# Performance work log

Hardware: AMD Instinct MI355X
Metric: run time of the kernel (lower is better)

## Reference

```python
import jax, jax.numpy as jnp
import numpy as np

B, C, T, W, H = 4, 128, 16, 64, 64


def setup_inputs() -> dict:
    key = jax.random.key(0)
    ks = jax.random.split(key, 5)
    Cq = C // 8
    return {
        "x": jax.random.normal(ks[0], (B, C, T, W, H), jnp.float32),
        # stacked params for the 3 cells (T, W, H order, as in nn.Sequential)
        "Wq": jax.random.normal(ks[1], (3, Cq, C), jnp.float32) * 0.05,
        "bq": jnp.zeros((3, Cq), jnp.float32),
        "Wk": jax.random.normal(ks[2], (3, Cq, C), jnp.float32) * 0.05,
        "bk": jnp.zeros((3, Cq), jnp.float32),
        "Wv": jax.random.normal(ks[3], (3, C, C), jnp.float32) * 0.05,
        "bv": jnp.zeros((3, C), jnp.float32),
        # gamma is init to 0 in torch (identity); small random so the test is nontrivial
        "gamma": jax.random.normal(ks[4], (3,), jnp.float32) * 0.1,
    }


def _conv1x1(x, w, b):
    # 1x1x1 Conv3d == channel contraction
    return jnp.einsum('bcthw,oc->bothw', x, w) + b[None, :, None, None, None]


def _cell(x, wq, bq, wk, bk, wv, bv, gamma, attn_dim):
    # Faithful to torch: raw contiguous .view() == row-major reshape.
    Bb, Cc, Tt, Ww, Hh = x.shape
    q = _conv1x1(x, wq, bq).reshape(Bb, attn_dim, -1)   # (B, A, N)
    k = _conv1x1(x, wk, bk).reshape(Bb, -1, attn_dim)   # (B, N, A)  (pooling_factor=1 -> MaxPool identity)
    attn = jax.nn.softmax(jnp.matmul(q, k), axis=-1)    # (B, A, A)
    v = _conv1x1(x, wv, bv).reshape(Bb, -1, attn_dim)   # (B, M, A), M = C*T*W*H/A
    out = jnp.matmul(v, attn.swapaxes(1, 2))            # (B, M, A)
    out = out.reshape(Bb, Cc, Ww, Hh, Tt).transpose(0, 1, 4, 2, 3)  # -> (B, C, T, W, H)
    return gamma * out + x


def reference(x, Wq, bq, Wk, bk, Wv, bv, gamma):
    _, _, Tt, Ww, Hh = x.shape
    attn_dims = (Tt, Ww, Hh)  # cells with attn_id 'T', 'W', 'H'
    for i in range(3):
        x = _cell(x, Wq[i], bq[i], Wk[i], bk[i], Wv[i], bv[i], gamma[i], attn_dims[i])
    return x
```

## Files before the change

kernel.cpp:

```cpp
#include <hip/hip_runtime.h>

#define BB 4
#define CC 128
#define CQ 16
#define TDIM 16
#define SS 65536
#define CS (CC*SS)
#define NBLK 256

typedef unsigned short u16;
typedef unsigned int   u32;

typedef __bf16 bf16x8v __attribute__((ext_vector_type(8)));
typedef float  floatx4v __attribute__((ext_vector_type(4)));

__device__ __forceinline__ u16 f2bf(float f) {
    u32 u = __float_as_uint(f);
    u32 r = (u + 0x7fffu + ((u >> 16) & 1u)) >> 16;
    return (u16)r;
}
__device__ __forceinline__ void unpack8(uint4 r, float* f) {
    f[0] = __uint_as_float(r.x << 16); f[1] = __uint_as_float(r.x & 0xffff0000u);
    f[2] = __uint_as_float(r.y << 16); f[3] = __uint_as_float(r.y & 0xffff0000u);
    f[4] = __uint_as_float(r.z << 16); f[5] = __uint_as_float(r.z & 0xffff0000u);
    f[6] = __uint_as_float(r.w << 16); f[7] = __uint_as_float(r.w & 0xffff0000u);
}
__device__ __forceinline__ bf16x8v ld_bf8(const void* p) {
    union { uint4 u; bf16x8v b; } x;
    x.u = *(const uint4*)p;
    return x.b;
}

__global__ __launch_bounds__(256) void wconv_kernel(
    const float* __restrict__ Wq, const float* __restrict__ Wk, const float* __restrict__ Wv,
    const float* __restrict__ bq, const float* __restrict__ bk, const float* __restrict__ bv,
    u16* __restrict__ wbf, float* __restrict__ bias)
{
    const int idx = blockIdx.x * 256 + threadIdx.x;
    const int cell = idx / 20480;
    const int j = idx - cell * 20480;
    const int o = j >> 7, c = j & 127;
    float v;
    if (o < 16)      v = Wq[(cell * 16 + o) * 128 + c];
    else if (o < 32) v = Wk[(cell * 16 + (o - 16)) * 128 + c];
    else             v = Wv[(cell * 128 + (o - 32)) * 128 + c];
    wbf[idx] = f2bf(v);
    if (idx < 480) {
        const int cl = idx / 160, oo = idx - cl * 160;
        float b = (oo < 16) ? bq[cl * 16 + oo]
                : (oo < 32) ? bk[cl * 16 + oo - 16]
                :             bv[cl * 128 + oo - 32];
        bias[idx] = b;
    }
}

__global__ __launch_bounds__(512, 4) void qkv_mfma_kernel(
    const float* __restrict__ x,
    const u16* __restrict__ wbf, const float* __restrict__ bias,
    float* __restrict__ qf, float* __restrict__ kf, u16* __restrict__ vf)
{
    __shared__ u16 xT[128 * 128];
    const int t  = threadIdx.x;
    const int b  = blockIdx.y;
    const int s0 = blockIdx.x << 7;
    const float* xb = x + (size_t)b * CS;

    {
        const int s4 = (t & 31) << 2;
        const int cr = t >> 5;
        const float* xs = xb + s0 + s4;
#pragma unroll
        for (int p = 0; p < 8; p++) {
            const int c = cr + p * 16;
            float4 f = *(const float4*)(xs + (size_t)c * SS);
            u16 h[4] = { f2bf(f.x), f2bf(f.y), f2bf(f.z), f2bf(f.w) };
#pragma unroll
            for (int j = 0; j < 4; j++) {
                const int sl = s4 + j;
                const u32 sw = (u32)(((sl & 7) ^ ((sl >> 3) & 7)) << 4);
                *(u16*)((char*)xT + ((((u32)sl << 8) + ((u32)c << 1)) ^ sw)) = h[j];
            }
        }
    }
    __syncthreads();

    const int lane = t & 63;
    const int wv   = t >> 6;
    const int mh   = wv >> 2;
    const int sq   = wv & 3;
    const int ln15 = lane & 15;
    const int lhi  = lane >> 4;

    floatx4v acc[5][2] = {};

    const u16* abase = wbf + ((mh * 80 + ln15) << 7) + (lhi << 3);

#pragma unroll
    for (int ks = 0; ks < 4; ks++) {
        bf16x8v af[5];
#pragma unroll
        for (int mi = 0; mi < 5; mi++)
            af[mi] = ld_bf8(abase + (mi << 11) + (ks << 5));
#pragma unroll
        for (int nt = 0; nt < 2; nt++) {
            const int sl = sq * 32 + nt * 16 + ln15;
            const u32 sw = (u32)(((sl & 7) ^ ((sl >> 3) & 7)) << 4);
            const u32 off = (((u32)sl << 8) + (u32)((ks << 6) + (lhi << 4))) ^ sw;
            bf16x8v bf = ld_bf8((const char*)xT + off);
#pragma unroll
            for (int mi = 0; mi < 5; mi++)
                acc[mi][nt] = __builtin_amdgcn_mfma_f32_16x16x32_bf16(
                                  af[mi], bf, acc[mi][nt], 0, 0, 0);
        }
    }

    float* qb = qf + (size_t)b * ((size_t)CQ * SS);
    float* kb = kf + (size_t)b * ((size_t)CQ * SS);
    u16*   vb = vf + (size_t)b * (size_t)CS;

    if (mh == 0) {
#pragma unroll
        for (int mi = 0; mi < 2; mi++) {
            const int o0 = mi * 16 + lhi * 4;
            float bia[4];
            *(float4*)bia = *(const float4*)(bias + o0);
            float* base = (mi == 0) ? qb : kb;
            const int row0 = o0 & 15;
#pragma unroll
            for (int nt = 0; nt < 2; nt++) {
                const int s = s0 + sq * 32 + nt * 16 + ln15;
#pragma unroll
                for (int r = 0; r < 4; r++)
                    base[(size_t)(row0 + r) * SS + s] = acc[mi][nt][r] + bia[r];
            }
        }
    }
    __syncthreads();

#pragma unroll
    for (int mi = 0; mi < 5; mi++) {
        const int o0 = mh * 80 + mi * 16 + lhi * 4;
        if (o0 >= 32) {
            float bia[4];
            *(float4*)bia = *(const float4*)(bias + o0);
            const int vc0 = o0 - 32;
#pragma unroll
            for (int nt = 0; nt < 2; nt++) {
                const int sl = sq * 32 + nt * 16 + ln15;
#pragma unroll
                for (int r = 0; r < 4; r++) {
                    const int vc = vc0 + r;
                    const u32 sw = (u32)(((vc & 7) ^ ((vc >> 3) & 7)) << 4);
                    *(u16*)((char*)xT + ((((u32)vc << 8) + ((u32)sl << 1)) ^ sw))
                        = f2bf(acc[mi][nt][r] + bia[r]);
                }
            }
        }
    }
    __syncthreads();

#pragma unroll
    for (int it = 0; it < 4; it++) {
        const int vc = (t >> 4) + it * 32;
        const u32 sw = (u32)(((vc & 7) ^ ((vc >> 3) & 7)) << 4);
        uint4 d = *(const uint4*)((char*)xT +
                      ((((u32)vc << 8) + ((u32)(t & 15) << 4)) ^ sw));
        *(uint4*)(vb + (size_t)vc * SS + s0 + ((t & 15) << 3)) = d;
    }
}

template <int A>
__global__ __launch_bounds__(256) void logits_part_kernel(
    const float* __restrict__ qf, const float* __restrict__ kf,
    float* __restrict__ part)
{
    constexpr int N = (CQ * SS) / A;
    constexpr int NCHUNK = N / NBLK;
    constexpr int NLOG = (NCHUNK == 64) ? 6 : 8;
    __shared__ float qs[A][NCHUNK + 1];
    __shared__ float ks[NCHUNK][A];
    const int t  = threadIdx.x;
    const int b  = blockIdx.y;
    const int n0 = blockIdx.x << NLOG;
    const float* qb = qf + (size_t)b * ((size_t)CQ * SS);
    const float* kb = kf + (size_t)b * ((size_t)CQ * SS);

    for (int idx = t; idx < A * NCHUNK; idx += 256) {
        int a1 = idx >> NLOG, n = idx & (NCHUNK - 1);
        qs[a1][n] = qb[(size_t)a1 * N + n0 + n];
    }
    float* ksf = &ks[0][0];
    for (int idx = t; idx < NCHUNK * A; idx += 256)
        ksf[idx] = kb[(size_t)n0 * A + idx];
    __syncthreads();

    float* pb = part + ((size_t)b * NBLK + blockIdx.x) * (A * A);

    if constexpr (A == 16) {
        int a1 = t >> 4, a2 = t & 15;
        float s = 0.f;
#pragma unroll 8
        for (int n = 0; n < NCHUNK; n++) s += qs[a1][n] * ks[n][a2];
        pb[t] = s;
    } else {
        int a1  = t & 63;
        int a2b = (t >> 6) * 16;
        float acc[16];
#pragma unroll
        for (int j = 0; j < 16; j++) acc[j] = 0.f;
        for (int n = 0; n < NCHUNK; n++) {
            float q = qs[a1][n];
#pragma unroll
            for (int j = 0; j < 16; j++) acc[j] += q * ks[n][a2b + j];
        }
        float* dst = pb + t * 16;
        *(float4*)(dst)      = make_float4(acc[0],  acc[1],  acc[2],  acc[3]);
        *(float4*)(dst + 4)  = make_float4(acc[4],  acc[5],  acc[6],  acc[7]);
        *(float4*)(dst + 8)  = make_float4(acc[8],  acc[9],  acc[10], acc[11]);
        *(float4*)(dst + 12) = make_float4(acc[12], acc[13], acc[14], acc[15]);
    }
}

template <int A>
__global__ __launch_bounds__(256) void reduce_softmax_kernel(
    const float* __restrict__ part, float* __restrict__ attn, u16* __restrict__ pbf)
{
    constexpr int NG = 256 / A;
    __shared__ float red[NG][A];
    const int a1 = blockIdx.x;
    const int b  = blockIdx.y;
    const int t  = threadIdx.x;
    const int a2 = t & (A - 1);
    const int g  = t >> ((A == 16) ? 4 : 6);
    const float* pb = part + (size_t)b * NBLK * (A * A);

    int off;
    if constexpr (A == 16) off = a1 * 16 + a2;
    else                   off = a1 * 16 + ((a2 >> 4) << 10) + (a2 & 15);

    float s0 = 0.f, s1 = 0.f, s2 = 0.f, s3 = 0.f;
    for (int blk = g; blk < NBLK; blk += 4 * NG) {
        s0 += pb[(size_t)(blk         ) * (A * A) + off];
        s1 += pb[(size_t)(blk +     NG) * (A * A) + off];
        s2 += pb[(size_t)(blk + 2 * NG) * (A * A) + off];
        s3 += pb[(size_t)(blk + 3 * NG) * (A * A) + off];
    }
    red[g][a2] = (s0 + s1) + (s2 + s3);
    __syncthreads();

    if (t < A) {
        float l = 0.f;
#pragma unroll
        for (int gg = 0; gg < NG; gg++) l += red[gg][t];
        float m = l;
#pragma unroll
        for (int o2 = A / 2; o2 > 0; o2 >>= 1) m = fmaxf(m, __shfl_xor(m, o2, 64));
        float e = expf(l - m);
        float s = e;
#pragma unroll
        for (int o2 = A / 2; o2 > 0; o2 >>= 1) s += __shfl_xor(s, o2, 64);
        const float p = e / s;
        attn[((size_t)b << 12) + a1 * A + t] = p;
        if constexpr (A == 64)
            pbf[((size_t)b << 12) + a1 * 64 + t] = f2bf(p);
    }
}

__global__ __launch_bounds__(256) void out16_kernel(
    const float* __restrict__ x, const u16* __restrict__ vf,
    const float* __restrict__ attn, const float* __restrict__ gptr,
    float* __restrict__ y)
{
    const int b = blockIdx.y;
    const u32 u = blockIdx.x * 256u + threadIdx.x;
    const float g = *gptr;
    const float* ab = attn + ((size_t)b << 12);
    const float* xb = x + (size_t)b * CS;
    float*       yb = y + (size_t)b * CS;
    const u16*   vr = vf + (size_t)b * CS + (size_t)u * 16;

    uint4 r0 = *(const uint4*)(vr);
    uint4 r1 = *(const uint4*)(vr + 8);
    float v0[8], v1[8];
    unpack8(r0, v0); unpack8(r1, v1);

    const size_t base = ((size_t)(u >> 12) << 16) + (u & 4095u);
#pragma unroll
    for (int tt = 0; tt < 16; tt++) {
        const float* ar = ab + tt * 16;
        float4 a0 = *(const float4*)(ar);
        float4 a1 = *(const float4*)(ar + 4);
        float4 a2 = *(const float4*)(ar + 8);
        float4 a3 = *(const float4*)(ar + 12);
        float acc = v0[0]*a0.x + v0[1]*a0.y + v0[2]*a0.z + v0[3]*a0.w
                  + v0[4]*a1.x + v0[5]*a1.y + v0[6]*a1.z + v0[7]*a1.w
                  + v1[0]*a2.x + v1[1]*a2.y + v1[2]*a2.z + v1[3]*a2.w
                  + v1[4]*a3.x + v1[5]*a3.y + v1[6]*a3.z + v1[7]*a3.w;
        const size_t i = base + ((size_t)tt << 12);
        yb[i] = g * acc + xb[i];
    }
}

__global__ __launch_bounds__(256) void out64_mfma_kernel(
    const float* __restrict__ x, const u16* __restrict__ vf,
    const u16* __restrict__ pbf, const float* __restrict__ gptr,
    float* __restrict__ y)
{
    const int b = blockIdx.y;
    const int t = threadIdx.x;
    const float g = *gptr;
    const int lane = t & 63;
    const int ln15 = lane & 15;
    const int lhi  = lane >> 4;
    const int wv   = t >> 6;
    const int m0w  = blockIdx.x * 256 + wv * 64;

    const u16*   pb = pbf + ((size_t)b << 12);
    const u16*   vb = vf + (size_t)b * CS;
    const float* xb = x + (size_t)b * CS;
    float*       yb = y + (size_t)b * CS;

    bf16x8v af[2][4];
#pragma unroll
    for (int ksi = 0; ksi < 2; ksi++)
#pragma unroll
        for (int sub = 0; sub < 4; sub++)
            af[ksi][sub] = ld_bf8(pb + (sub * 16 + ln15) * 64 + ksi * 32 + lhi * 8);

#pragma unroll
    for (int tile = 0; tile < 4; tile++) {
        const int m0 = m0w + tile * 16;
        const u16* vrow = vb + ((size_t)(m0 + ln15) << 6) + (lhi << 3);
        bf16x8v b0 = ld_bf8(vrow);
        bf16x8v b1 = ld_bf8(vrow + 32);

        floatx4v acc[4] = {};
#pragma unroll
        for (int sub = 0; sub < 4; sub++) {
            acc[sub] = __builtin_amdgcn_mfma_f32_16x16x32_bf16(af[0][sub], b0, acc[sub], 0, 0, 0);
            acc[sub] = __builtin_amdgcn_mfma_f32_16x16x32_bf16(af[1][sub], b1, acc[sub], 0, 0, 0);
        }

        const int c   = m0 >> 10;
        const int ow  = ((m0 >> 6) & 15) * 4 + ((m0 & 63) >> 4);
        const size_t base = ((size_t)c << 16) + ((size_t)ow << 6) + (size_t)(ln15 << 2);
        const float* xbase = xb + base;
        float*       ybase = yb + base;
#pragma unroll
        for (int r = 0; r < 4; r++) {
            const int ot = lhi * 4 + r;
            float4 xv = *(const float4*)(xbase + ((size_t)ot << 12));
            float4 o;
            o.x = g * acc[0][r] + xv.x;
            o.y = g * acc[1][r] + xv.y;
            o.z = g * acc[2][r] + xv.z;
            o.w = g * acc[3][r] + xv.w;
            *(float4*)(ybase + ((size_t)ot << 12)) = o;
        }
    }
}

extern "C" void kernel_launch(void* const* d_in, const int* in_sizes, int n_in,
                              void* d_out, int out_size, void* d_ws, size_t ws_size,
                              hipStream_t stream)
{
    (void)in_sizes; (void)n_in; (void)out_size;
    const float* x0    = (const float*)d_in[0];
    const float* Wq    = (const float*)d_in[1];
    const float* bq    = (const float*)d_in[2];
    const float* Wk    = (const float*)d_in[3];
    const float* bk    = (const float*)d_in[4];
    const float* Wv    = (const float*)d_in[5];
    const float* bv    = (const float*)d_in[6];
    const float* gamma = (const float*)d_in[7];
    float* y = (float*)d_out;

    const size_t MiB = (size_t)1 << 20;
    const size_t need4 = 4 * (28 * MiB + 16384 + 8192) + 160 * 128 * 3 * 2 + 3 * 160 * 4;
    const int nb = (ws_size >= need4) ? 4 : 1;

    char* ws = (char*)d_ws;
    float* qf    = (float*)ws;
    float* kf    = (float*)(ws + (size_t)nb * 4  * MiB);
    u16*   vf    = (u16*)  (ws + (size_t)nb * 8  * MiB);
    float* part  = (float*)(ws + (size_t)nb * 24 * MiB);
    float* attnp = (float*)(ws + (size_t)nb * 28 * MiB);
    u16*   pbf   = (u16*)  (ws + (size_t)nb * 28 * MiB + (size_t)nb * 16384);
    u16*   wbf3  = (u16*)  (ws + (size_t)nb * 28 * MiB + (size_t)nb * (16384 + 8192));
    float* bias3 = (float*)(ws + (size_t)nb * 28 * MiB + (size_t)nb * (16384 + 8192)
                               + 160 * 128 * 3 * 2);

    wconv_kernel<<<240, 256, 0, stream>>>(Wq, Wk, Wv, bq, bk, bv, wbf3, bias3);

    for (int cell = 0; cell < 3; cell++) {
        const u16*   wc = wbf3  + (size_t)cell * 160 * 128;
        const float* bc = bias3 + (size_t)cell * 160;
        for (int b0 = 0; b0 < BB; b0 += nb) {
            const float* xin = ((cell == 0) ? x0 : (const float*)y) + (size_t)b0 * CS;
            float* yb = y + (size_t)b0 * CS;

            qkv_mfma_kernel<<<dim3(512, nb), 512, 0, stream>>>(xin, wc, bc, qf, kf, vf);

            if (cell == 0) {
                logits_part_kernel<16><<<dim3(NBLK, nb), 256, 0, stream>>>(qf, kf, part);
                reduce_softmax_kernel<16><<<dim3(16, nb), 256, 0, stream>>>(part, attnp, pbf);
                out16_kernel<<<dim3(2048, nb), 256, 0, stream>>>(xin, vf, attnp, gamma + cell, yb);
            } else {
                logits_part_kernel<64><<<dim3(NBLK, nb), 256, 0, stream>>>(qf, kf, part);
                reduce_softmax_kernel<64><<<dim3(64, nb), 256, 0, stream>>>(part, attnp, pbf);
                out64_mfma_kernel<<<dim3(512, nb), 256, 0, stream>>>(xin, vf, pbf, gamma + cell, yb);
            }
        }
    }
}
```

Before: 626.9 us.

## Halve qkv tile to 64 positions with 256-thread blocks and packed LDS stores

The QKV projection kernel now handles 64 spatial positions per block with 256 threads instead of 128 positions with 512 threads, doubling the grid and raising the occupancy hint. The x load is restructured so each thread reads 8 channels as scalar strided loads, packs them to bf16 and writes one 16-byte swizzled LDS store instead of many 2-byte scattered stores. The LDS swizzle is simplified to match the smaller tile. The host also adds an nb=2 fallback for workspace sizing. The tradeoffs are scalar global loads instead of float4 and twice as many weight-fragment loads per output position.

```diff
diff --git a/kernel.cpp b/kernel.cpp
--- a/kernel.cpp
+++ b/kernel.cpp
@@ -54,40 +54,43 @@
     }
 }
 
-__global__ __launch_bounds__(512, 4) void qkv_mfma_kernel(
+__global__ __launch_bounds__(256, 8) void qkv_mfma_kernel(
     const float* __restrict__ x,
     const u16* __restrict__ wbf, const float* __restrict__ bias,
     float* __restrict__ qf, float* __restrict__ kf, u16* __restrict__ vf)
 {
-    __shared__ u16 xT[128 * 128];
+    __shared__ u16 xT[64 * 128];
     const int t  = threadIdx.x;
     const int b  = blockIdx.y;
-    const int s0 = blockIdx.x << 7;
+    const int s0 = blockIdx.x << 6;
     const float* xb = x + (size_t)b * CS;
 
     {
-        const int s4 = (t & 31) << 2;
-        const int cr = t >> 5;
-        const float* xs = xb + s0 + s4;
-#pragma unroll
-        for (int p = 0; p < 8; p++) {
-            const int c = cr + p * 16;
-            float4 f = *(const float4*)(xs + (size_t)c * SS);
-            u16 h[4] = { f2bf(f.x), f2bf(f.y), f2bf(f.z), f2bf(f.w) };
-#pragma unroll
-            for (int j = 0; j < 4; j++) {
-                const int sl = s4 + j;
-                const u32 sw = (u32)(((sl & 7) ^ ((sl >> 3) & 7)) << 4);
-                *(u16*)((char*)xT + ((((u32)sl << 8) + ((u32)c << 1)) ^ sw)) = h[j];
-            }
+        const int sl = t & 63;
+        const int ob = t >> 6;
+        const float* xs = xb + s0 + sl;
+        const u32 rowb = (u32)sl << 8;
+        const u32 swz  = (u32)(sl & 7) << 4;
+#pragma unroll
+        for (int p = 0; p < 4; p++) {
+            const int c0 = (ob + p * 4) << 3;
+            float f[8];
+#pragma unroll
+            for (int j = 0; j < 8; j++) f[j] = xs[(size_t)(c0 + j) * SS];
+            uint4 pk;
+            pk.x = (u32)f2bf(f[0]) | ((u32)f2bf(f[1]) << 16);
+            pk.y = (u32)f2bf(f[2]) | ((u32)f2bf(f[3]) << 16);
+            pk.z = (u32)f2bf(f[4]) | ((u32)f2bf(f[5]) << 16);
+            pk.w = (u32)f2bf(f[6]) | ((u32)f2bf(f[7]) << 16);
+            *(uint4*)((char*)xT + ((rowb + (u32)(c0 << 1)) ^ swz)) = pk;
         }
     }
     __syncthreads();
 
     const int lane = t & 63;
     const int wv   = t >> 6;
-    const int mh   = wv >> 2;
-    const int sq   = wv & 3;
+    const int mh   = wv >> 1;
+    const int sh   = wv & 1;
     const int ln15 = lane & 15;
     const int lhi  = lane >> 4;
 
@@ -103,9 +106,9 @@
             af[mi] = ld_bf8(abase + (mi << 11) + (ks << 5));
 #pragma unroll
         for (int nt = 0; nt < 2; nt++) {
-            const int sl = sq * 32 + nt * 16 + ln15;
-            const u32 sw = (u32)(((sl & 7) ^ ((sl >> 3) & 7)) << 4);
-            const u32 off = (((u32)sl << 8) + (u32)((ks << 6) + (lhi << 4))) ^ sw;
+            const int sl = sh * 32 + nt * 16 + ln15;
+            const u32 off = (((u32)sl << 8) + (u32)((ks << 6) + (lhi << 4)))
+                          ^ ((u32)(ln15 & 7) << 4);
             bf16x8v bf = ld_bf8((const char*)xT + off);
 #pragma unroll
             for (int mi = 0; mi < 5; mi++)
@@ -128,7 +131,7 @@
             const int row0 = o0 & 15;
 #pragma unroll
             for (int nt = 0; nt < 2; nt++) {
-                const int s = s0 + sq * 32 + nt * 16 + ln15;
+                const int s = s0 + sh * 32 + nt * 16 + ln15;
 #pragma unroll
                 for (int r = 0; r < 4; r++)
                     base[(size_t)(row0 + r) * SS + s] = acc[mi][nt][r] + bia[r];
@@ -146,12 +149,12 @@
             const int vc0 = o0 - 32;
 #pragma unroll
             for (int nt = 0; nt < 2; nt++) {
-                const int sl = sq * 32 + nt * 16 + ln15;
+                const int sl = sh * 32 + nt * 16 + ln15;
 #pragma unroll
                 for (int r = 0; r < 4; r++) {
                     const int vc = vc0 + r;
-                    const u32 sw = (u32)(((vc & 7) ^ ((vc >> 3) & 7)) << 4);
-                    *(u16*)((char*)xT + ((((u32)vc << 8) + ((u32)sl << 1)) ^ sw))
+                    *(u16*)((char*)xT + ((((u32)vc << 7) + ((u32)sl << 1))
+                                         ^ ((u32)(vc & 7) << 4)))
                         = f2bf(acc[mi][nt][r] + bia[r]);
                 }
             }
@@ -161,11 +164,11 @@
 
 #pragma unroll
     for (int it = 0; it < 4; it++) {
-        const int vc = (t >> 4) + it * 32;
-        const u32 sw = (u32)(((vc & 7) ^ ((vc >> 3) & 7)) << 4);
+        const int vc  = (t >> 3) + it * 32;
+        const int col = t & 7;
         uint4 d = *(const uint4*)((char*)xT +
-                      ((((u32)vc << 8) + ((u32)(t & 15) << 4)) ^ sw));
-        *(uint4*)(vb + (size_t)vc * SS + s0 + ((t & 15) << 3)) = d;
+                      ((((u32)vc << 7) + ((u32)col << 4)) ^ ((u32)(vc & 7) << 4)));
+        *(uint4*)(vb + (size_t)vc * SS + s0 + (col << 3)) = d;
     }
 }
 
@@ -376,8 +379,11 @@
     float* y = (float*)d_out;
 
     const size_t MiB = (size_t)1 << 20;
-    const size_t need4 = 4 * (28 * MiB + 16384 + 8192) + 160 * 128 * 3 * 2 + 3 * 160 * 4;
-    const int nb = (ws_size >= need4) ? 4 : 1;
+    const size_t WTAB = (size_t)160 * 128 * 3 * 2 + 480 * 4;
+    auto need = [&](int nbv) -> size_t {
+        return (size_t)nbv * (28 * MiB + 16384 + 8192) + WTAB;
+    };
+    const int nb = (ws_size >= need(4)) ? 4 : (ws_size >= need(2)) ? 2 : 1;
 
     char* ws = (char*)d_ws;
     float* qf    = (float*)ws;
@@ -387,8 +393,7 @@
     float* attnp = (float*)(ws + (size_t)nb * 28 * MiB);
     u16*   pbf   = (u16*)  (ws + (size_t)nb * 28 * MiB + (size_t)nb * 16384);
     u16*   wbf3  = (u16*)  (ws + (size_t)nb * 28 * MiB + (size_t)nb * (16384 + 8192));
-    float* bias3 = (float*)(ws + (size_t)nb * 28 * MiB + (size_t)nb * (16384 + 8192)
-                               + 160 * 128 * 3 * 2);
+    float* bias3 = (float*)((char*)wbf3 + (size_t)160 * 128 * 3 * 2);
 
     wconv_kernel<<<240, 256, 0, stream>>>(Wq, Wk, Wv, bq, bk, bv, wbf3, bias3);
 
@@ -399,7 +404,7 @@
             const float* xin = ((cell == 0) ? x0 : (const float*)y) + (size_t)b0 * CS;
             float* yb = y + (size_t)b0 * CS;
 
-            qkv_mfma_kernel<<<dim3(512, nb), 512, 0, stream>>>(xin, wc, bc, qf, kf, vf);
+            qkv_mfma_kernel<<<dim3(1024, nb), 256, 0, stream>>>(xin, wc, bc, qf, kf, vf);
 
             if (cell == 0) {
                 logits_part_kernel<16><<<dim3(NBLK, nb), 256, 0, stream>>>(qf, kf, part);
```

New measurement: 979.6 us. 56.3% more time.
